# Kernel tuning notes

Hardware: AMD Instinct MI355X
Metric: run time of the kernel (lower is better)

## Reference

```python
import jax, jax.numpy as jnp
import numpy as np
from jax import lax

C = 256        # CONV_DIM / hidden size
VOC = 97       # VOC_SIZE + 1
T_DEC = 25     # NUM_CHARS
N = 512        # number of rois
H_IN, W_IN = 8, 32
GROUPS = 32    # GroupNorm groups (detectron2 'GN' default)


def setup_inputs() -> dict:
    key = jax.random.key(0)
    ks = jax.random.split(key, 16)
    nrm = lambda k, shp, s=0.05: jax.random.normal(k, shp, dtype=jnp.float32) * s
    inp = {}
    inp['rois'] = jax.random.normal(ks[0], (N, C, H_IN, W_IN), dtype=jnp.float32)
    inp['targets'] = jax.random.randint(ks[1], (N, T_DEC), 0, VOC)
    inp['conv1_w'] = nrm(ks[2], (C, C, 3, 3))
    inp['gn1_s'] = jnp.ones((C,), jnp.float32); inp['gn1_b'] = jnp.zeros((C,), jnp.float32)
    inp['conv2_w'] = nrm(ks[3], (C, C, 3, 3))
    inp['gn2_s'] = jnp.ones((C,), jnp.float32); inp['gn2_b'] = jnp.zeros((C,), jnp.float32)
    inp['lstm_wih_f'] = nrm(ks[4], (4 * C, C)); inp['lstm_whh_f'] = nrm(ks[5], (4 * C, C))
    inp['lstm_bih_f'] = jnp.zeros((4 * C,), jnp.float32); inp['lstm_bhh_f'] = jnp.zeros((4 * C,), jnp.float32)
    inp['lstm_wih_b'] = nrm(ks[6], (4 * C, C)); inp['lstm_whh_b'] = nrm(ks[7], (4 * C, C))
    inp['lstm_bih_b'] = jnp.zeros((4 * C,), jnp.float32); inp['lstm_bhh_b'] = jnp.zeros((4 * C,), jnp.float32)
    inp['emb_w'] = nrm(ks[8], (C, 2 * C)); inp['emb_b'] = jnp.zeros((C,), jnp.float32)
    inp['att_emb'] = nrm(ks[9], (VOC, C), 1.0)
    inp['comb_w'] = nrm(ks[10], (C, 2 * C)); inp['comb_b'] = jnp.zeros((C,), jnp.float32)
    inp['gru_wih'] = nrm(ks[11], (3 * C, C)); inp['gru_whh'] = nrm(ks[12], (3 * C, C))
    inp['gru_bih'] = jnp.zeros((3 * C,), jnp.float32); inp['gru_bhh'] = jnp.zeros((3 * C,), jnp.float32)
    inp['out_w'] = nrm(ks[13], (VOC, C)); inp['out_b'] = jnp.zeros((VOC,), jnp.float32)
    inp['vat_w'] = nrm(ks[14], (1, C)); inp['vat_b'] = jnp.zeros((1,), jnp.float32)
    return inp


def group_norm(x, scale, bias, groups=GROUPS, eps=1e-5):
    n, c, h, w = x.shape
    xg = x.reshape(n, groups, c // groups, h, w)
    mu = xg.mean(axis=(2, 3, 4), keepdims=True)
    var = xg.var(axis=(2, 3, 4), keepdims=True)
    xg = (xg - mu) * lax.rsqrt(var + eps)
    return xg.reshape(n, c, h, w) * scale[None, :, None, None] + bias[None, :, None, None]


def lstm_dir(xs, w_ih, w_hh, b_ih, b_hh, reverse):
    # xs: (T, N, C); PyTorch LSTM gate order i, f, g, o
    n = xs.shape[1]; hdim = w_hh.shape[1]
    def step(carry, x):
        h, c = carry
        g = x @ w_ih.T + b_ih + h @ w_hh.T + b_hh
        i, f, gg, o = jnp.split(g, 4, axis=-1)
        c = jax.nn.sigmoid(f) * c + jax.nn.sigmoid(i) * jnp.tanh(gg)
        h = jax.nn.sigmoid(o) * jnp.tanh(c)
        return (h, c), h
    z = jnp.zeros((n, hdim), xs.dtype)
    _, hs = lax.scan(step, (z, z), xs, reverse=reverse)
    return hs


def reference(rois, targets, conv1_w, gn1_s, gn1_b, conv2_w, gn2_s, gn2_b,
              lstm_wih_f, lstm_whh_f, lstm_bih_f, lstm_bhh_f,
              lstm_wih_b, lstm_whh_b, lstm_bih_b, lstm_bhh_b,
              emb_w, emb_b, att_emb, comb_w, comb_b,
              gru_wih, gru_whh, gru_bih, gru_bhh, out_w, out_b, vat_w, vat_b):
    # ---- CRNN encoder ----
    def conv_gn_relu(x, w, s, b):
        y = lax.conv_general_dilated(x, w, window_strides=(2, 1),
                                     padding=((1, 1), (1, 1)),
                                     dimension_numbers=('NCHW', 'OIHW', 'NCHW'))
        return jax.nn.relu(group_norm(y, s, b))
    x = conv_gn_relu(rois, conv1_w, gn1_s, gn1_b)
    x = conv_gn_relu(x, conv2_w, gn2_s, gn2_b)
    x = x.mean(axis=2).transpose(2, 0, 1)            # (T=W, N, C)
    hf = lstm_dir(x, lstm_wih_f, lstm_whh_f, lstm_bih_f, lstm_bhh_f, False)
    hb = lstm_dir(x, lstm_wih_b, lstm_whh_b, lstm_bih_b, lstm_bhh_b, True)
    enc = jnp.concatenate([hf, hb], axis=-1) @ emb_w.T + emb_b   # (T, N, C)

    # ---- attention GRU decoder (training path, deterministic teacher forcing) ----
    n = enc.shape[1]
    dec_in = jnp.concatenate([jnp.zeros((n, 1), targets.dtype), targets[:, :-1]], axis=1).T  # (T_DEC, N)
    dec_tgt = targets.T                                                                        # (T_DEC, N)

    def dec_step(h, inp):
        tok, tgt = inp                       # (N,), (N,)
        emb = att_emb[tok]                   # (N, C); dropout disabled
        alpha = jnp.tanh(h[None] + enc)      # (T, N, C)
        scores = jnp.einsum('tnc,c->tn', alpha, vat_w[0]) + vat_b[0]
        aw = jax.nn.softmax(scores, axis=0)  # softmax over encoder time
        ctx = jnp.einsum('tn,tnc->nc', aw, enc)
        xin = jax.nn.relu(jnp.concatenate([emb, ctx], axis=1) @ comb_w.T + comb_b)
        gi = xin @ gru_wih.T + gru_bih
        gh = h @ gru_whh.T + gru_bhh
        ir, iz, inn = jnp.split(gi, 3, axis=1)
        hr, hz, hn = jnp.split(gh, 3, axis=1)
        r = jax.nn.sigmoid(ir + hr)
        z = jax.nn.sigmoid(iz + hz)
        ng = jnp.tanh(inn + r * hn)
        h_new = (1.0 - z) * ng + z * h
        logp = jax.nn.log_softmax(h_new @ out_w.T + out_b, axis=1)
        step_loss = -jnp.mean(jnp.take_along_axis(logp, tgt[:, None], axis=1))
        return h_new, step_loss

    h0 = jnp.zeros((n, C), enc.dtype)
    _, losses = lax.scan(dec_step, h0, (dec_in, dec_tgt))
    return losses.sum()
```

## Files before the change

kernel.cpp:

```cpp
#include <hip/hip_runtime.h>
#include <math.h>

#define NROI 512
#define CDIM 256
#define TENC 32
#define TDEC 25
#define VOCC 97

typedef unsigned short ushort_t;
typedef unsigned char uchar_t;
typedef __attribute__((ext_vector_type(8))) short short8v;
typedef __attribute__((ext_vector_type(4))) float float4v;

__device__ __forceinline__ float sigmoidf_(float x){
    x = fminf(fmaxf(x, -30.f), 30.f);
    return __builtin_amdgcn_rcpf(1.f + __expf(-x));
}
__device__ __forceinline__ float tanhf_(float x){
    x = fminf(fmaxf(x, -15.f), 15.f);
    float e = __expf(2.f * x);
    return (e - 1.f) * __builtin_amdgcn_rcpf(e + 1.f);
}
__device__ __forceinline__ ushort_t f2b(float f){
    unsigned u = __float_as_uint(f);
    u = u + 0x7fffu + ((u >> 16) & 1u);
    return (ushort_t)(u >> 16);
}
__device__ __forceinline__ float b2f(ushort_t h){
    return __uint_as_float(((unsigned)h) << 16);
}
__device__ __forceinline__ uchar_t f2fp8(float x){
    x = fminf(fmaxf(x, -448.f), 448.f);
    int p = __builtin_amdgcn_cvt_pk_fp8_f32(x, x, 0, false);
    return (uchar_t)(p & 0xff);
}

__global__ void convert_all_k(
    const float* c1s, const float* c2s, const float* wf, const float* wb,
    const float* hf, const float* hb, const float* em, const float* cb,
    const float* gi, const float* gh, const float* ow, const float* ob,
    const float* bif, const float* bhf, const float* bib, const float* bhb,
    ushort_t* d_c1, ushort_t* d_c2, ushort_t* d_wf, ushort_t* d_wb,
    uchar_t* d_hf8, uchar_t* d_hb8, ushort_t* d_em,
    ushort_t* d_cwL, uchar_t* d_cwR8,
    uchar_t* d_gi8, uchar_t* d_gh8, ushort_t* d_ow, float* d_ob,
    float* d_b2f, float* d_b2b)
{
    int i = blockIdx.x * 256 + threadIdx.x;
    if (i < 589824) {
        int co = i / 2304, rem = i % 2304, tap = rem >> 8, ci = rem & 255;
        d_c1[i] = f2b(c1s[co * 2304 + ci * 9 + tap]); return;
    }
    i -= 589824;
    if (i < 589824) {
        int co = i / 2304, rem = i % 2304, tap = rem >> 8, ci = rem & 255;
        d_c2[i] = f2b(c2s[co * 2304 + ci * 9 + tap]); return;
    }
    i -= 589824;
    if (i < 262144) { d_wf[i] = f2b(wf[i]); return; }  i -= 262144;
    if (i < 262144) { d_wb[i] = f2b(wb[i]); return; }  i -= 262144;
    if (i < 262144) { d_hf8[i] = f2fp8(hf[i]); return; }  i -= 262144;
    if (i < 262144) { d_hb8[i] = f2fp8(hb[i]); return; }  i -= 262144;
    if (i < 131072) { d_em[i] = f2b(em[i]); return; }  i -= 131072;
    if (i < 131072) {
        int col = i >> 9, rest = i & 511;
        float v = cb[i];
        if (rest < 256) d_cwL[col * 256 + rest] = f2b(v);
        else            d_cwR8[col * 256 + (rest - 256)] = f2fp8(v);
        return;
    }
    i -= 131072;
    if (i < 196608) { d_gi8[i] = f2fp8(gi[i]); return; }  i -= 196608;
    if (i < 196608) { d_gh8[i] = f2fp8(gh[i]); return; }  i -= 196608;
    if (i < 32768) {
        int r = i >> 8;
        d_ow[i] = (r < VOCC) ? f2b(ow[i - (r << 8) + r * 256]) : 0; return;
    }
    i -= 32768;
    if (i < 128) { d_ob[i] = (i < VOCC) ? ob[i] : 0.f; return; }  i -= 128;
    if (i < 1024) { d_b2f[i] = bif[i] + bhf[i]; return; }  i -= 1024;
    if (i < 1024) { d_b2b[i] = bib[i] + bhb[i]; return; }
}

__global__ void nchw2nhwc_k(const float* __restrict__ in, ushort_t* __restrict__ out)
{
    __shared__ float t[64][33];
    int b = blockIdx.x;
    int cb = b & 3, h = (b >> 2) & 7, n = b >> 5;
    const float* src = in + (((size_t)n * 256 + cb * 64) * 8 + h) * 32;
    int w = threadIdx.x & 31, cr = threadIdx.x >> 5;
    #pragma unroll
    for (int p = 0; p < 8; p++) {
        int c = p * 8 + cr;
        t[c][w] = src[(size_t)c * 256 + w];
    }
    __syncthreads();
    int c2 = threadIdx.x & 63, wr2 = threadIdx.x >> 6;
    ushort_t* dst = out + ((size_t)n * 8 + h) * 32 * 256 + cb * 64;
    #pragma unroll
    for (int q = 0; q < 8; q++) {
        int ww = q * 4 + wr2;
        dst[(size_t)ww * 256 + c2] = f2b(t[c2][ww]);
    }
}

__global__ void emb_gather_k(const int* __restrict__ targets, const float* __restrict__ att_emb,
                             ushort_t* __restrict__ EMB)
{
    int idx = blockIdx.x * 256 + threadIdx.x;
    int c = idx & 255;
    int n = (idx >> 8) & 511;
    int t = idx >> 17;
    int tok = (t == 0) ? 0 : targets[n * TDEC + t - 1];
    EMB[idx] = f2b(att_emb[tok * 256 + c]);
}

template<int OUTBF, int ACT>
__global__ void __launch_bounds__(256, 2)
mgemm_k(const ushort_t* __restrict__ A, const ushort_t* __restrict__ B,
        const float* __restrict__ bias, void* __restrict__ Cout,
        int M, int N, int K)
{
    __shared__ ushort_t As[128 * 40];
    __shared__ ushort_t Bs[128 * 40];
    const int tid = threadIdx.x;
    const int lane = tid & 63, wid = tid >> 6;
    const int wr = wid >> 1, wc = wid & 1;
    const int bm = blockIdx.y * 128, bn = blockIdx.x * 128;

    const int r0 = tid >> 2, c0 = tid & 3;
    const int r1 = r0 + 64;
    const size_t Ar0 = (size_t)(bm + r0) * K, Ar1 = (size_t)(bm + r1) * K;
    const size_t Br0 = (size_t)(bn + r0) * K, Br1 = (size_t)(bn + r1) * K;

    float4v acc[4][4];
    #pragma unroll
    for (int m = 0; m < 4; m++)
        #pragma unroll
        for (int n = 0; n < 4; n++) { float4v z = {0.f,0.f,0.f,0.f}; acc[m][n] = z; }

    short8v ra[2][2], rb[2][2];
    auto LOAD = [&](int b, int k0) {
        ra[b][0] = *(const short8v*)&A[Ar0 + k0 + c0 * 8];
        ra[b][1] = *(const short8v*)&A[Ar1 + k0 + c0 * 8];
        rb[b][0] = *(const short8v*)&B[Br0 + k0 + c0 * 8];
        rb[b][1] = *(const short8v*)&B[Br1 + k0 + c0 * 8];
    };
    auto STORE = [&](int b) {
        *(short8v*)&As[r0 * 40 + c0 * 8] = ra[b][0];
        *(short8v*)&As[r1 * 40 + c0 * 8] = ra[b][1];
        *(short8v*)&Bs[r0 * 40 + c0 * 8] = rb[b][0];
        *(short8v*)&Bs[r1 * 40 + c0 * 8] = rb[b][1];
    };
    const int lr = lane & 15, lk = lane >> 4;
    auto COMPUTE = [&]() {
        short8v af[4], bf[4];
        #pragma unroll
        for (int m = 0; m < 4; m++)
            af[m] = *(const short8v*)&As[(wr * 64 + m * 16 + lr) * 40 + lk * 8];
        #pragma unroll
        for (int n = 0; n < 4; n++)
            bf[n] = *(const short8v*)&Bs[(wc * 64 + n * 16 + lr) * 40 + lk * 8];
        #pragma unroll
        for (int m = 0; m < 4; m++)
            #pragma unroll
            for (int n = 0; n < 4; n++)
                acc[m][n] = __builtin_amdgcn_mfma_f32_16x16x32_bf16(af[m], bf[n], acc[m][n], 0, 0, 0);
    };

    LOAD(0, 0);
    for (int k0 = 0; k0 < K; k0 += 64) {
        __syncthreads();
        STORE(0);
        __syncthreads();
        LOAD(1, k0 + 32);
        COMPUTE();
        __syncthreads();
        STORE(1);
        __syncthreads();
        if (k0 + 64 < K) LOAD(0, k0 + 64);
        COMPUTE();
    }

    #pragma unroll
    for (int m = 0; m < 4; m++)
        #pragma unroll
        for (int n = 0; n < 4; n++)
            #pragma unroll
            for (int r = 0; r < 4; r++) {
                int row = bm + wr * 64 + m * 16 + lk * 4 + r;
                int col = bn + wc * 64 + n * 16 + lr;
                float v = acc[m][n][r];
                if (bias) v += bias[col];
                if (ACT == 1) v = fmaxf(v, 0.f);
                if (OUTBF) ((ushort_t*)Cout)[(size_t)row * N + col] = f2b(v);
                else       ((float*)   Cout)[(size_t)row * N + col] = v;
            }
}

template<int CONV2>
__global__ void __launch_bounds__(256, 2)
convf_k(const ushort_t* __restrict__ in, const ushort_t* __restrict__ wt,
        const float* __restrict__ gns, const float* __restrict__ gnb,
        ushort_t* __restrict__ out, int Hin, int hmask, int nshift)
{
    const int K = 2304;
    __shared__ ushort_t As[128 * 40];
    __shared__ ushort_t Bs[256 * 40];
    const int tid = threadIdx.x;
    const int lane = tid & 63, wv = tid >> 6;
    const int byy = (blockIdx.y & 7) * (gridDim.y >> 3) + (blockIdx.y >> 3);
    const int bm = byy * 128;

    const int r0 = tid >> 2, c0 = tid & 3;
    const int r1 = r0 + 64;
    const int row0 = bm + r0, row1 = bm + r1;
    const int wo0 = row0 & 31, wo1 = row1 & 31;
    const int hh0 = ((row0 >> 5) & hmask) * 2 - 1, hh1 = ((row1 >> 5) & hmask) * 2 - 1;
    const size_t base0 = (size_t)(row0 >> nshift) * Hin * 32 * 256;
    const size_t base1 = (size_t)(row1 >> nshift) * Hin * 32 * 256;
    size_t Br[4];
    #pragma unroll
    for (int j = 0; j < 4; j++) Br[j] = (size_t)(r0 + j * 64) * K;

    float4v acc[8][4];
    #pragma unroll
    for (int m = 0; m < 8; m++)
        #pragma unroll
        for (int n = 0; n < 4; n++) { float4v z = {0.f,0.f,0.f,0.f}; acc[m][n] = z; }

    short8v ra[2][2], rb[2][4];
    const short8v zv = {0,0,0,0,0,0,0,0};
    auto LOAD = [&](int b, int k0) {
        int tap = k0 >> 8;
        int kh = tap / 3, kw = tap - kh * 3;
        int ci = (k0 & 255) + c0 * 8;
        int hi0 = hh0 + kh, wi0 = wo0 - 1 + kw;
        int hi1 = hh1 + kh, wi1 = wo1 - 1 + kw;
        ra[b][0] = ((unsigned)hi0 < (unsigned)Hin && (unsigned)wi0 < 32u)
                 ? *(const short8v*)&in[base0 + ((size_t)hi0 * 32 + wi0) * 256 + ci] : zv;
        ra[b][1] = ((unsigned)hi1 < (unsigned)Hin && (unsigned)wi1 < 32u)
                 ? *(const short8v*)&in[base1 + ((size_t)hi1 * 32 + wi1) * 256 + ci] : zv;
        #pragma unroll
        for (int j = 0; j < 4; j++)
            rb[b][j] = *(const short8v*)&wt[Br[j] + k0 + c0 * 8];
    };
    auto STORE = [&](int b) {
        *(short8v*)&As[r0 * 40 + c0 * 8] = ra[b][0];
        *(short8v*)&As[r1 * 40 + c0 * 8] = ra[b][1];
        #pragma unroll
        for (int j = 0; j < 4; j++)
            *(short8v*)&Bs[(r0 + j * 64) * 40 + c0 * 8] = rb[b][j];
    };
    const int lr = lane & 15, lk = lane >> 4;
    auto COMPUTE = [&]() {
        short8v af[8];
        #pragma unroll
        for (int m = 0; m < 8; m++)
            af[m] = *(const short8v*)&As[(m * 16 + lr) * 40 + lk * 8];
        #pragma unroll
        for (int n = 0; n < 4; n++) {
            short8v bf = *(const short8v*)&Bs[(wv * 64 + n * 16 + lr) * 40 + lk * 8];
            #pragma unroll
            for (int m = 0; m < 8; m++)
                acc[m][n] = __builtin_amdgcn_mfma_f32_16x16x32_bf16(af[m], bf, acc[m][n], 0, 0, 0);
        }
    };

    LOAD(0, 0);
    for (int k0 = 0; k0 < K; k0 += 64) {
        __syncthreads();
        STORE(0);
        __syncthreads();
        LOAD(1, k0 + 32);
        COMPUTE();
        __syncthreads();
        STORE(1);
        __syncthreads();
        if (k0 + 64 < K) LOAD(0, k0 + 64);
        COMPUTE();
    }

    float sc_[4], bb_[4];
    #pragma unroll
    for (int nn = 0; nn < 4; nn++) {
        int col = wv * 64 + nn * 16 + lr;
        sc_[nn] = gns[col];
        bb_[nn] = gnb[col];
    }

    if (CONV2 == 0) {
        float mu_[4], rs_[4];
        #pragma unroll
        for (int nn = 0; nn < 4; nn++) {
            float s = 0.f, q = 0.f;
            #pragma unroll
            for (int m = 0; m < 8; m++)
                #pragma unroll
                for (int r = 0; r < 4; r++) { float v = acc[m][nn][r]; s += v; q += v * v; }
            s += __shfl_xor(s, 16); q += __shfl_xor(q, 16);
            s += __shfl_xor(s, 32); q += __shfl_xor(q, 32);
            s += __shfl_xor(s, 1);  q += __shfl_xor(q, 1);
            s += __shfl_xor(s, 2);  q += __shfl_xor(q, 2);
            s += __shfl_xor(s, 4);  q += __shfl_xor(q, 4);
            float mu = s * (1.f / 1024.f);
            mu_[nn] = mu;
            rs_[nn] = rsqrtf(q * (1.f / 1024.f) - mu * mu + 1e-5f);
        }
        #pragma unroll
        for (int m = 0; m < 8; m++)
            #pragma unroll
            for (int nn = 0; nn < 4; nn++)
                #pragma unroll
                for (int r = 0; r < 4; r++) {
                    int row = bm + m * 16 + lk * 4 + r;
                    int col = wv * 64 + nn * 16 + lr;
                    float v = (acc[m][nn][r] - mu_[nn]) * rs_[nn] * sc_[nn] + bb_[nn];
                    out[(size_t)row * 256 + col] = f2b(fmaxf(v, 0.f));
                }
    } else {
        float mu_[2][4], rs_[2][4];
        #pragma unroll
        for (int img = 0; img < 2; img++)
            #pragma unroll
            for (int nn = 0; nn < 4; nn++) {
                float s = 0.f, q = 0.f;
                #pragma unroll
                for (int m2 = 0; m2 < 4; m2++)
                    #pragma unroll
                    for (int r = 0; r < 4; r++) {
                        float v = acc[img * 4 + m2][nn][r]; s += v; q += v * v;
                    }
                s += __shfl_xor(s, 16); q += __shfl_xor(q, 16);
                s += __shfl_xor(s, 32); q += __shfl_xor(q, 32);
                s += __shfl_xor(s, 1);  q += __shfl_xor(q, 1);
                s += __shfl_xor(s, 2);  q += __shfl_xor(q, 2);
                s += __shfl_xor(s, 4);  q += __shfl_xor(q, 4);
                float mu = s * (1.f / 512.f);
                mu_[img][nn] = mu;
                rs_[img][nn] = rsqrtf(q * (1.f / 512.f) - mu * mu + 1e-5f);
            }
        const int nimg0 = bm >> 6;
        #pragma unroll
        for (int img = 0; img < 2; img++)
            #pragma unroll
            for (int m2 = 0; m2 < 2; m2++)
                #pragma unroll
                for (int nn = 0; nn < 4; nn++)
                    #pragma unroll
                    for (int r = 0; r < 4; r++) {
                        int m = img * 4 + m2;
                        float v0 = (acc[m][nn][r]     - mu_[img][nn]) * rs_[img][nn] * sc_[nn] + bb_[nn];
                        float v1 = (acc[m + 2][nn][r] - mu_[img][nn]) * rs_[img][nn] * sc_[nn] + bb_[nn];
                        float pooled = 0.5f * (fmaxf(v0, 0.f) + fmaxf(v1, 0.f));
                        int wo = m2 * 16 + lk * 4 + r;
                        int nimg = nimg0 + img;
                        int col = wv * 64 + nn * 16 + lr;
                        out[((size_t)wo * 512 + nimg) * 256 + col] = f2b(pooled);
                    }
    }
}

__global__ void __launch_bounds__(512, 1)
lstm_persist_k(const ushort_t* __restrict__ XG,
               const uchar_t* __restrict__ whF8, const uchar_t* __restrict__ whB8,
               ushort_t* __restrict__ hcat)
{
    __shared__ __align__(16) uchar_t hf8[16][264];
    __shared__ float gL[16][1028];
    const int blk = blockIdx.x;
    const int dir = blk >> 5;
    const int r0  = (blk & 31) * 16;
    const uchar_t* W = dir ? whB8 : whF8;
    const int tid = threadIdx.x, lane = tid & 63, wv = tid >> 6;
    const int lr = lane & 15, lk = lane >> 4;
    const float4v z4 = {0.f, 0.f, 0.f, 0.f};

    long pw[8][8];
    #pragma unroll
    for (int j = 0; j < 8; j++) {
        int col0 = (j * 8 + wv) * 16;
        #pragma unroll
        for (int kf = 0; kf < 8; kf++)
            pw[j][kf] = *(const long*)&W[(size_t)(col0 + lr) * 256 + kf * 32 + lk * 8];
    }

    for (int i = tid; i < 16 * 264; i += 512) ((uchar_t*)hf8)[i] = 0;
    float creg[8];
    #pragma unroll
    for (int r = 0; r < 8; r++) creg[r] = 0.f;
    const int ccol = tid & 255;
    const int rbase = (tid >> 8) * 8;
    __syncthreads();

    for (int s = 0; s < TENC; s++) {
        int t = dir ? (31 - s) : s;
        float xga[8][4];
        #pragma unroll
        for (int j = 0; j < 8; j++) {
            int col = (j * 8 + wv) * 16 + lr;
            #pragma unroll
            for (int r = 0; r < 4; r++)
                xga[j][r] = b2f(XG[(size_t)t * 1048576 +
                                   (size_t)(r0 + lk * 4 + r) * 2048 + dir * 1024 + col]);
        }
        long aH[8];
        #pragma unroll
        for (int kf = 0; kf < 8; kf++)
            aH[kf] = *(const long*)&hf8[lr][kf * 32 + lk * 8];
        #pragma unroll
        for (int j = 0; j < 8; j++) {
            int col = (j * 8 + wv) * 16 + lr;
            float4v acc = z4;
            #pragma unroll
            for (int kf = 0; kf < 8; kf++)
                acc = __builtin_amdgcn_mfma_f32_16x16x32_fp8_fp8(aH[kf], pw[j][kf], acc, 0, 0, 0);
            #pragma unroll
            for (int r = 0; r < 4; r++)
                gL[lk * 4 + r][col] = acc[r] + xga[j][r];
        }
        __syncthreads();
        #pragma unroll
        for (int rr = 0; rr < 8; rr++) {
            int row = rbase + rr;
            float i_ = sigmoidf_(gL[row][ccol]);
            float f_ = sigmoidf_(gL[row][256 + ccol]);
            float g_ = tanhf_(gL[row][512 + ccol]);
            float o_ = sigmoidf_(gL[row][768 + ccol]);
            float cn = f_ * creg[rr] + i_ * g_;
            creg[rr] = cn;
            float hn = o_ * tanhf_(cn);
            hf8[row][ccol] = f2fp8(hn);
            hcat[((size_t)t * 512 + (r0 + row)) * 512 + dir * 256 + ccol] = f2b(hn);
        }
        __syncthreads();
    }
}

__global__ void __launch_bounds__(512, 1)
dec_local_k(const ushort_t* __restrict__ enc, const ushort_t* __restrict__ xinpre,
            const uchar_t* __restrict__ cwR8, const uchar_t* __restrict__ gwih8,
            const uchar_t* __restrict__ gwhh8, const float* __restrict__ gbih,
            const float* __restrict__ gbhh, const float* __restrict__ vw,
            const float* __restrict__ vb, ushort_t* __restrict__ hist)
{
    __shared__ ushort_t encL[2][32][264];
    __shared__ __align__(16) uchar_t cwL8[16 * 8 * 64 * 8];
    __shared__ float    hL[2][256];
    __shared__ __align__(16) uchar_t hf8[2][264];
    __shared__ __align__(16) uchar_t xf8[2][264];
    __shared__ __align__(16) uchar_t ctx8[2][264];
    __shared__ float    giL[2][776];
    __shared__ float    ghL[2][776];
    __shared__ float    scl[2][32];

    const int tid = threadIdx.x, lane = tid & 63, wv = tid >> 6;
    const int nbase = blockIdx.x * 2;
    const int lr = lane & 15, lk = lane >> 4;
    const float4v z4 = {0.f,0.f,0.f,0.f};

    for (int i = tid; i < 2 * 256; i += 512) hL[i >> 8][i & 255] = 0.f;
    for (int i = tid; i < 2 * 264; i += 512) hf8[i / 264][i % 264] = 0;
    for (int v = tid; v < 2048; v += 512) {
        int r = v >> 10;
        int rem = v & 1023;
        int t2 = rem >> 5;
        int c8 = (rem & 31) * 8;
        *(short8v*)&encL[r][t2][c8] =
            *(const short8v*)&enc[((size_t)t2 * 512 + nbase + r) * 256 + c8];
    }
    #pragma unroll
    for (int q = 0; q < 2; q++) {
        int tile = wv * 2 + q;
        int col0 = tile * 16;
        #pragma unroll
        for (int kf = 0; kf < 8; kf++) {
            long v = *(const long*)&cwR8[(size_t)(col0 + lr) * 256 + kf * 32 + lk * 8];
            *(long*)&cwL8[((tile * 8 + kf) * 64 + lane) * 8] = v;
        }
    }
    long pgh[6][8], pgi[6][8];
    #pragma unroll
    for (int j = 0; j < 6; j++) {
        int col0 = (j * 8 + wv) * 16;
        #pragma unroll
        for (int kf = 0; kf < 8; kf++) {
            pgh[j][kf] = *(const long*)&gwhh8[(size_t)(col0 + lr) * 256 + kf * 32 + lk * 8];
            pgi[j][kf] = *(const long*)&gwih8[(size_t)(col0 + lr) * 256 + kf * 32 + lk * 8];
        }
    }
    __syncthreads();

    float vwreg[4];
    #pragma unroll
    for (int j = 0; j < 4; j++) vwreg[j] = vw[lane + 64 * j];
    const float vbias = vb[0];
    float gbh_r[6], gbi_r[6];
    #pragma unroll
    for (int j = 0; j < 6; j++) {
        int col0 = (j * 8 + wv) * 16;
        gbh_r[j] = gbhh[col0 + lr];
        gbi_r[j] = gbih[col0 + lr];
    }

    for (int t = 0; t < TDEC; t++) {
        float xp[2][2];
        #pragma unroll
        for (int q = 0; q < 2; q++) {
            int col0 = (wv * 2 + q) * 16;
            xp[q][0] = b2f(xinpre[(size_t)t * 131072 + (size_t)(nbase + 0) * 256 + col0 + lr]);
            xp[q][1] = b2f(xinpre[(size_t)t * 131072 + (size_t)(nbase + 1) * 256 + col0 + lr]);
        }
        float4v ghacc[6];
        {
            long aH[8];
            #pragma unroll
            for (int kf = 0; kf < 8; kf++)
                aH[kf] = (lr < 2) ? *(const long*)&hf8[lr][kf * 32 + lk * 8] : 0L;
            #pragma unroll
            for (int j = 0; j < 6; j++) {
                float4v acc = z4;
                #pragma unroll
                for (int kf = 0; kf < 8; kf++)
                    acc = __builtin_amdgcn_mfma_f32_16x16x32_fp8_fp8(aH[kf], pgh[j][kf], acc, 0, 0, 0);
                ghacc[j] = acc;
            }
        }
        {
            int r = wv >> 2;
            int t2b = (wv & 3) * 8;
            float hreg[4];
            #pragma unroll
            for (int j = 0; j < 4; j++) hreg[j] = hL[r][lane + 64 * j];
            #pragma unroll
            for (int q = 0; q < 8; q++) {
                int t2 = t2b + q;
                float s = 0.f;
                #pragma unroll
                for (int j = 0; j < 4; j++)
                    s += tanhf_(hreg[j] + b2f(encL[r][t2][lane + 64 * j])) * vwreg[j];
                for (int o = 32; o > 0; o >>= 1) s += __shfl_down(s, o);
                if (lane == 0) scl[r][t2] = s + vbias;
            }
        }
        if (lk == 0) {
            #pragma unroll
            for (int j = 0; j < 6; j++) {
                int col0 = (j * 8 + wv) * 16;
                ghL[0][col0 + lr] = ghacc[j][0] + gbh_r[j];
                ghL[1][col0 + lr] = ghacc[j][1] + gbh_r[j];
            }
        }
        __syncthreads();
        {
            int r = tid >> 8, c = tid & 255;
            float m = -1e30f;
            #pragma unroll
            for (int t2 = 0; t2 < 32; t2++) m = fmaxf(m, scl[r][t2]);
            float ssum = 0.f, acc = 0.f;
            #pragma unroll 8
            for (int t2 = 0; t2 < 32; t2++) {
                float e = __expf(scl[r][t2] - m);
                ssum += e;
                acc += e * b2f(encL[r][t2][c]);
            }
            ctx8[r][c] = f2fp8(acc * __builtin_amdgcn_rcpf(ssum));
        }
        __syncthreads();
        {
            long aC[8];
            #pragma unroll
            for (int kf = 0; kf < 8; kf++)
                aC[kf] = (lr < 2) ? *(const long*)&ctx8[lr][kf * 32 + lk * 8] : 0L;
            #pragma unroll
            for (int q = 0; q < 2; q++) {
                int tile = wv * 2 + q;
                int col0 = tile * 16;
                float4v acc = z4;
                #pragma unroll
                for (int kf = 0; kf < 8; kf++) {
                    long b = *(const long*)&cwL8[((tile * 8 + kf) * 64 + lane) * 8];
                    acc = __builtin_amdgcn_mfma_f32_16x16x32_fp8_fp8(aC[kf], b, acc, 0, 0, 0);
                }
                if (lk == 0) {
                    xf8[0][col0 + lr] = f2fp8(fmaxf(acc[0] + xp[q][0], 0.f));
                    xf8[1][col0 + lr] = f2fp8(fmaxf(acc[1] + xp[q][1], 0.f));
                }
            }
        }
        __syncthreads();
        {
            long aX[8];
            #pragma unroll
            for (int kf = 0; kf < 8; kf++)
                aX[kf] = (lr < 2) ? *(const long*)&xf8[lr][kf * 32 + lk * 8] : 0L;
            #pragma unroll
            for (int j = 0; j < 6; j++) {
                int col0 = (j * 8 + wv) * 16;
                float4v acc = z4;
                #pragma unroll
                for (int kf = 0; kf < 8; kf++)
                    acc = __builtin_amdgcn_mfma_f32_16x16x32_fp8_fp8(aX[kf], pgi[j][kf], acc, 0, 0, 0);
                if (lk == 0) {
                    giL[0][col0 + lr] = acc[0] + gbi_r[j];
                    giL[1][col0 + lr] = acc[1] + gbi_r[j];
                }
            }
        }
        __syncthreads();
        {
            int r = tid >> 8, c = tid & 255;
            float rg = sigmoidf_(giL[r][c] + ghL[r][c]);
            float zg = sigmoidf_(giL[r][256 + c] + ghL[r][256 + c]);
            float ng = tanhf_(giL[r][512 + c] + rg * ghL[r][512 + c]);
            float hv = (1.f - zg) * ng + zg * hL[r][c];
            hL[r][c] = hv;
            hf8[r][c] = f2fp8(hv);
            __builtin_nontemporal_store(f2b(hv), &hist[((size_t)t * 512 + nbase + r) * 256 + c]);
        }
        __syncthreads();
    }
}

__global__ void loss_batch_k(const float* __restrict__ logits, const int* __restrict__ targets,
                             float* __restrict__ part)
{
    __shared__ float red[256];
    int t = blockIdx.x;
    float acc = 0.f;
    for (int rr = threadIdx.x; rr < 512; rr += 256) {
        const float* row = logits + ((size_t)t * 512 + rr) * 128;
        float m = -1e30f;
        for (int j = 0; j < VOCC; j++) m = fmaxf(m, row[j]);
        float s2 = 0.f;
        for (int j = 0; j < VOCC; j++) s2 += __expf(row[j] - m);
        int tg = targets[rr * TDEC + t];
        acc += m + __logf(s2) - row[tg];
    }
    red[threadIdx.x] = acc;
    __syncthreads();
    for (int o = 128; o > 0; o >>= 1) {
        if (threadIdx.x < o) red[threadIdx.x] += red[threadIdx.x + o];
        __syncthreads();
    }
    if (threadIdx.x == 0) part[t] = red[0] / 512.f;
}

__global__ void loss_final_k(const float* __restrict__ part, float* __restrict__ out)
{
    if (threadIdx.x == 0) {
        float s = 0.f;
        for (int t = 0; t < TDEC; t++) s += part[t];
        out[0] = s;
    }
}

extern "C" void kernel_launch(void* const* d_in, const int* in_sizes, int n_in,
                              void* d_out, int out_size, void* d_ws, size_t ws_size,
                              hipStream_t stream)
{
    const float* rois     = (const float*)d_in[0];
    const int*   targets  = (const int*)  d_in[1];
    const float* conv1_w  = (const float*)d_in[2];
    const float* gn1_s    = (const float*)d_in[3];
    const float* gn1_b    = (const float*)d_in[4];
    const float* conv2_w  = (const float*)d_in[5];
    const float* gn2_s    = (const float*)d_in[6];
    const float* gn2_b    = (const float*)d_in[7];
    const float* wih_f    = (const float*)d_in[8];
    const float* whh_f    = (const float*)d_in[9];
    const float* bih_f    = (const float*)d_in[10];
    const float* bhh_f    = (const float*)d_in[11];
    const float* wih_b    = (const float*)d_in[12];
    const float* whh_b    = (const float*)d_in[13];
    const float* bih_b    = (const float*)d_in[14];
    const float* bhh_b    = (const float*)d_in[15];
    const float* emb_w    = (const float*)d_in[16];
    const float* emb_b    = (const float*)d_in[17];
    const float* att_emb  = (const float*)d_in[18];
    const float* comb_w   = (const float*)d_in[19];
    const float* comb_b   = (const float*)d_in[20];
    const float* gru_wih  = (const float*)d_in[21];
    const float* gru_whh  = (const float*)d_in[22];
    const float* gru_bih  = (const float*)d_in[23];
    const float* gru_bhh  = (const float*)d_in[24];
    const float* out_w    = (const float*)d_in[25];
    const float* out_b    = (const float*)d_in[26];
    const float* vat_w    = (const float*)d_in[27];
    const float* vat_b    = (const float*)d_in[28];

    float* ws = (float*)d_ws;
    const size_t REG1 = 0;
    const size_t REG2 = 16777216;
    const size_t REG3 = 25165824;
    const size_t WREG = 33554432;

    ushort_t* R      = (ushort_t*)(ws + REG1);
    ushort_t* xg     = (ushort_t*)(ws + REG1);
    ushort_t* EMB    = (ushort_t*)(ws + REG1);
    ushort_t* xinpre = (ushort_t*)(ws + REG1 + 1638400);

    ushort_t* xT     = (ushort_t*)(ws + REG2 + 4194304);
    ushort_t* hcat   = (ushort_t*)(ws + REG2);
    ushort_t* X1b    = (ushort_t*)(ws + REG3);
    ushort_t* enc    = (ushort_t*)(ws + REG3);
    ushort_t* hist   = (ushort_t*)(ws + REG3 + 2097152);
    float*    logitsA= ws + REG3 + 3735552;
    float*    lpart  = ws + REG3 + 5373952;

    ushort_t* c1w    = (ushort_t*)(ws + WREG);
    ushort_t* c2w    = (ushort_t*)(ws + WREG + 294912);
    ushort_t* wihf   = (ushort_t*)(ws + WREG + 589824);
    uchar_t*  whhf8  = (uchar_t*) (ws + WREG + 851968);
    uchar_t*  whhb8  = (uchar_t*) (ws + WREG + 917504);
    ushort_t* embw   = (ushort_t*)(ws + WREG + 1114112);
    ushort_t* cwL    = (ushort_t*)(ws + WREG + 1179648);
    uchar_t*  cwR8   = (uchar_t*) (ws + WREG + 1212416);
    uchar_t*  gwih8  = (uchar_t*) (ws + WREG + 1245184);
    uchar_t*  gwhh8  = (uchar_t*) (ws + WREG + 1294336);
    ushort_t* outw   = (ushort_t*)(ws + WREG + 1343488);
    float*    outb   = ws + WREG + 1359872;
    float*    bias2f = ws + WREG + 1360000;
    float*    bias2b = ws + WREG + 1361024;

    dim3 blk(256);

    convert_all_k<<<11402, blk, 0, stream>>>(
        conv1_w, conv2_w, wih_f, wih_b, whh_f, whh_b, emb_w, comb_w,
        gru_wih, gru_whh, out_w, out_b, bih_f, bhh_f, bih_b, bhh_b,
        c1w, c2w, wihf, (ushort_t*)(ws + WREG + 720896), whhf8, whhb8, embw,
        cwL, cwR8, gwih8, gwhh8, outw, outb, bias2f, bias2b);

    nchw2nhwc_k<<<16384, blk, 0, stream>>>(rois, R);
    convf_k<0><<<dim3(1, 512), blk, 0, stream>>>(R, c1w, gn1_s, gn1_b, X1b, 8, 3, 7);
    convf_k<1><<<dim3(1, 256), blk, 0, stream>>>(X1b, c2w, gn2_s, gn2_b, xT, 4, 1, 6);

    mgemm_k<1,0><<<dim3(16, 128), blk, 0, stream>>>(xT, wihf, bias2f, xg, 16384, 2048, 256);

    lstm_persist_k<<<64, dim3(512), 0, stream>>>(xg, whhf8, whhb8, hcat);

    mgemm_k<1,0><<<dim3(2, 128), blk, 0, stream>>>(hcat, embw, emb_b, enc, 16384, 256, 512);

    emb_gather_k<<<12800, blk, 0, stream>>>(targets, att_emb, EMB);
    mgemm_k<1,0><<<dim3(2, 100), blk, 0, stream>>>(EMB, cwL, comb_b, xinpre, 12800, 256, 256);

    dec_local_k<<<256, dim3(512), 0, stream>>>(enc, xinpre, cwR8, gwih8, gwhh8,
        gru_bih, gru_bhh, vat_w, vat_b, hist);

    mgemm_k<0,0><<<dim3(1, 100), blk, 0, stream>>>(hist, outw, outb, logitsA, 12800, 128, 256);
    loss_batch_k<<<TDEC, blk, 0, stream>>>(logitsA, targets, lpart);
    loss_final_k<<<1, dim3(64), 0, stream>>>(lpart, (float*)d_out);
}
```

Measured before the change: 719.3 us.

## Spread LSTM and GRU decoder recurrences over more blocks with fewer rows each

The persistent LSTM kernel now handles 4 ROI rows per block across 256 blocks instead of 16 rows across 64 blocks. The GRU attention decoder now handles one ROI per block across 512 blocks instead of two per block across 256. The goal is to cut the length of each block's serial recurrence and spread the work over more compute units of the MI355X. In exchange, each MFMA tile carries more zero padding, half the threads sit idle in the elementwise phases, and every block reloads the recurrent weights into registers, which adds more weight traffic overall. The decoder's launch bound changes from (512,1) to (512,4), which could force register spilling given the large per-thread weight arrays.

Measured after the change: 775.7 us. +7.8%, slower.

```diff
diff --git a/kernel.cpp b/kernel.cpp
--- a/kernel.cpp
+++ b/kernel.cpp
@@ -366,11 +366,11 @@
                const uchar_t* __restrict__ whF8, const uchar_t* __restrict__ whB8,
                ushort_t* __restrict__ hcat)
 {
-    __shared__ __align__(16) uchar_t hf8[16][264];
-    __shared__ float gL[16][1028];
+    __shared__ __align__(16) uchar_t hf8[4][264];
+    __shared__ float gL[4][1028];
     const int blk = blockIdx.x;
-    const int dir = blk >> 5;
-    const int r0  = (blk & 31) * 16;
+    const int dir = blk >> 7;
+    const int r0  = (blk & 127) * 4;
     const uchar_t* W = dir ? whB8 : whF8;
     const int tid = threadIdx.x, lane = tid & 63, wv = tid >> 6;
     const int lr = lane & 15, lk = lane >> 4;
@@ -385,29 +385,30 @@
             pw[j][kf] = *(const long*)&W[(size_t)(col0 + lr) * 256 + kf * 32 + lk * 8];
     }
 
-    for (int i = tid; i < 16 * 264; i += 512) ((uchar_t*)hf8)[i] = 0;
-    float creg[8];
-    #pragma unroll
-    for (int r = 0; r < 8; r++) creg[r] = 0.f;
+    for (int i = tid; i < 4 * 264; i += 512) ((uchar_t*)hf8)[i] = 0;
+    float creg[2];
+    creg[0] = 0.f; creg[1] = 0.f;
     const int ccol = tid & 255;
-    const int rbase = (tid >> 8) * 8;
+    const int rbase = (tid >> 8) * 2;
     __syncthreads();
 
     for (int s = 0; s < TENC; s++) {
         int t = dir ? (31 - s) : s;
         float xga[8][4];
-        #pragma unroll
-        for (int j = 0; j < 8; j++) {
-            int col = (j * 8 + wv) * 16 + lr;
-            #pragma unroll
-            for (int r = 0; r < 4; r++)
-                xga[j][r] = b2f(XG[(size_t)t * 1048576 +
-                                   (size_t)(r0 + lk * 4 + r) * 2048 + dir * 1024 + col]);
+        if (lk == 0) {
+            #pragma unroll
+            for (int j = 0; j < 8; j++) {
+                int col = (j * 8 + wv) * 16 + lr;
+                #pragma unroll
+                for (int r = 0; r < 4; r++)
+                    xga[j][r] = b2f(XG[(size_t)t * 1048576 +
+                                       (size_t)(r0 + r) * 2048 + dir * 1024 + col]);
+            }
         }
         long aH[8];
         #pragma unroll
         for (int kf = 0; kf < 8; kf++)
-            aH[kf] = *(const long*)&hf8[lr][kf * 32 + lk * 8];
+            aH[kf] = (lr < 4) ? *(const long*)&hf8[lr][kf * 32 + lk * 8] : 0L;
         #pragma unroll
         for (int j = 0; j < 8; j++) {
             int col = (j * 8 + wv) * 16 + lr;
@@ -415,13 +416,15 @@
             #pragma unroll
             for (int kf = 0; kf < 8; kf++)
                 acc = __builtin_amdgcn_mfma_f32_16x16x32_fp8_fp8(aH[kf], pw[j][kf], acc, 0, 0, 0);
-            #pragma unroll
-            for (int r = 0; r < 4; r++)
-                gL[lk * 4 + r][col] = acc[r] + xga[j][r];
-        }
-        __syncthreads();
-        #pragma unroll
-        for (int rr = 0; rr < 8; rr++) {
+            if (lk == 0) {
+                #pragma unroll
+                for (int r = 0; r < 4; r++)
+                    gL[r][col] = acc[r] + xga[j][r];
+            }
+        }
+        __syncthreads();
+        #pragma unroll
+        for (int rr = 0; rr < 2; rr++) {
             int row = rbase + rr;
             float i_ = sigmoidf_(gL[row][ccol]);
             float f_ = sigmoidf_(gL[row][256 + ccol]);
@@ -437,37 +440,35 @@
     }
 }
 
-__global__ void __launch_bounds__(512, 1)
+__global__ void __launch_bounds__(512, 4)
 dec_local_k(const ushort_t* __restrict__ enc, const ushort_t* __restrict__ xinpre,
             const uchar_t* __restrict__ cwR8, const uchar_t* __restrict__ gwih8,
             const uchar_t* __restrict__ gwhh8, const float* __restrict__ gbih,
             const float* __restrict__ gbhh, const float* __restrict__ vw,
             const float* __restrict__ vb, ushort_t* __restrict__ hist)
 {
-    __shared__ ushort_t encL[2][32][264];
+    __shared__ ushort_t encL[32][264];
     __shared__ __align__(16) uchar_t cwL8[16 * 8 * 64 * 8];
-    __shared__ float    hL[2][256];
-    __shared__ __align__(16) uchar_t hf8[2][264];
-    __shared__ __align__(16) uchar_t xf8[2][264];
-    __shared__ __align__(16) uchar_t ctx8[2][264];
-    __shared__ float    giL[2][776];
-    __shared__ float    ghL[2][776];
-    __shared__ float    scl[2][32];
+    __shared__ float    hL[256];
+    __shared__ __align__(16) uchar_t hf8[264];
+    __shared__ __align__(16) uchar_t xf8[264];
+    __shared__ __align__(16) uchar_t ctx8[264];
+    __shared__ float    giL[776];
+    __shared__ float    ghL[776];
+    __shared__ float    scl[32];
 
     const int tid = threadIdx.x, lane = tid & 63, wv = tid >> 6;
-    const int nbase = blockIdx.x * 2;
+    const int n = blockIdx.x;
     const int lr = lane & 15, lk = lane >> 4;
     const float4v z4 = {0.f,0.f,0.f,0.f};
 
-    for (int i = tid; i < 2 * 256; i += 512) hL[i >> 8][i & 255] = 0.f;
-    for (int i = tid; i < 2 * 264; i += 512) hf8[i / 264][i % 264] = 0;
-    for (int v = tid; v < 2048; v += 512) {
-        int r = v >> 10;
-        int rem = v & 1023;
-        int t2 = rem >> 5;
-        int c8 = (rem & 31) * 8;
-        *(short8v*)&encL[r][t2][c8] =
-            *(const short8v*)&enc[((size_t)t2 * 512 + nbase + r) * 256 + c8];
+    for (int i = tid; i < 256; i += 512) hL[i] = 0.f;
+    for (int i = tid; i < 264; i += 512) hf8[i] = 0;
+    for (int v = tid; v < 1024; v += 512) {
+        int t2 = v >> 5;
+        int c8 = (v & 31) * 8;
+        *(short8v*)&encL[t2][c8] =
+            *(const short8v*)&enc[((size_t)t2 * 512 + n) * 256 + c8];
     }
     #pragma unroll
     for (int q = 0; q < 2; q++) {
@@ -504,19 +505,18 @@
     }
 
     for (int t = 0; t < TDEC; t++) {
-        float xp[2][2];
+        float xp[2];
         #pragma unroll
         for (int q = 0; q < 2; q++) {
             int col0 = (wv * 2 + q) * 16;
-            xp[q][0] = b2f(xinpre[(size_t)t * 131072 + (size_t)(nbase + 0) * 256 + col0 + lr]);
-            xp[q][1] = b2f(xinpre[(size_t)t * 131072 + (size_t)(nbase + 1) * 256 + col0 + lr]);
+            xp[q] = b2f(xinpre[(size_t)t * 131072 + (size_t)n * 256 + col0 + lr]);
         }
         float4v ghacc[6];
         {
             long aH[8];
             #pragma unroll
             for (int kf = 0; kf < 8; kf++)
-                aH[kf] = (lr < 2) ? *(const long*)&hf8[lr][kf * 32 + lk * 8] : 0L;
+                aH[kf] = (lr == 0) ? *(const long*)&hf8[kf * 32 + lk * 8] : 0L;
             #pragma unroll
             for (int j = 0; j < 6; j++) {
                 float4v acc = z4;
@@ -527,51 +527,49 @@
             }
         }
         {
-            int r = wv >> 2;
-            int t2b = (wv & 3) * 8;
+            int t2b = wv * 4;
             float hreg[4];
             #pragma unroll
-            for (int j = 0; j < 4; j++) hreg[j] = hL[r][lane + 64 * j];
-            #pragma unroll
-            for (int q = 0; q < 8; q++) {
+            for (int j = 0; j < 4; j++) hreg[j] = hL[lane + 64 * j];
+            #pragma unroll
+            for (int q = 0; q < 4; q++) {
                 int t2 = t2b + q;
                 float s = 0.f;
                 #pragma unroll
                 for (int j = 0; j < 4; j++)
-                    s += tanhf_(hreg[j] + b2f(encL[r][t2][lane + 64 * j])) * vwreg[j];
+                    s += tanhf_(hreg[j] + b2f(encL[t2][lane + 64 * j])) * vwreg[j];
                 for (int o = 32; o > 0; o >>= 1) s += __shfl_down(s, o);
-                if (lane == 0) scl[r][t2] = s + vbias;
+                if (lane == 0) scl[t2] = s + vbias;
             }
         }
         if (lk == 0) {
             #pragma unroll
             for (int j = 0; j < 6; j++) {
                 int col0 = (j * 8 + wv) * 16;
-                ghL[0][col0 + lr] = ghacc[j][0] + gbh_r[j];
-                ghL[1][col0 + lr] = ghacc[j][1] + gbh_r[j];
-            }
-        }
-        __syncthreads();
-        {
-            int r = tid >> 8, c = tid & 255;
+                ghL[col0 + lr] = ghacc[j][0] + gbh_r[j];
+            }
+        }
+        __syncthreads();
+        if (tid < 256) {
+            int c = tid;
             float m = -1e30f;
             #pragma unroll
-            for (int t2 = 0; t2 < 32; t2++) m = fmaxf(m, scl[r][t2]);
+            for (int t2 = 0; t2 < 32; t2++) m = fmaxf(m, scl[t2]);
             float ssum = 0.f, acc = 0.f;
             #pragma unroll 8
             for (int t2 = 0; t2 < 32; t2++) {
-                float e = __expf(scl[r][t2] - m);
+                float e = __expf(scl[t2] - m);
                 ssum += e;
-                acc += e * b2f(encL[r][t2][c]);
-            }
-            ctx8[r][c] = f2fp8(acc * __builtin_amdgcn_rcpf(ssum));
+                acc += e * b2f(encL[t2][c]);
+            }
+            ctx8[c] = f2fp8(acc * __builtin_amdgcn_rcpf(ssum));
         }
         __syncthreads();
         {
             long aC[8];
             #pragma unroll
             for (int kf = 0; kf < 8; kf++)
-                aC[kf] = (lr < 2) ? *(const long*)&ctx8[lr][kf * 32 + lk * 8] : 0L;
+                aC[kf] = (lr == 0) ? *(const long*)&ctx8[kf * 32 + lk * 8] : 0L;
             #pragma unroll
             for (int q = 0; q < 2; q++) {
                 int tile = wv * 2 + q;
@@ -582,10 +580,8 @@
                     long b = *(const long*)&cwL8[((tile * 8 + kf) * 64 + lane) * 8];
                     acc = __builtin_amdgcn_mfma_f32_16x16x32_fp8_fp8(aC[kf], b, acc, 0, 0, 0);
                 }
-                if (lk == 0) {
-                    xf8[0][col0 + lr] = f2fp8(fmaxf(acc[0] + xp[q][0], 0.f));
-                    xf8[1][col0 + lr] = f2fp8(fmaxf(acc[1] + xp[q][1], 0.f));
-                }
+                if (lk == 0)
+                    xf8[col0 + lr] = f2fp8(fmaxf(acc[0] + xp[q], 0.f));
             }
         }
         __syncthreads();
@@ -593,7 +589,7 @@
             long aX[8];
             #pragma unroll
             for (int kf = 0; kf < 8; kf++)
-                aX[kf] = (lr < 2) ? *(const long*)&xf8[lr][kf * 32 + lk * 8] : 0L;
+                aX[kf] = (lr == 0) ? *(const long*)&xf8[kf * 32 + lk * 8] : 0L;
             #pragma unroll
             for (int j = 0; j < 6; j++) {
                 int col0 = (j * 8 + wv) * 16;
@@ -601,22 +597,20 @@
                 #pragma unroll
                 for (int kf = 0; kf < 8; kf++)
                     acc = __builtin_amdgcn_mfma_f32_16x16x32_fp8_fp8(aX[kf], pgi[j][kf], acc, 0, 0, 0);
-                if (lk == 0) {
-                    giL[0][col0 + lr] = acc[0] + gbi_r[j];
-                    giL[1][col0 + lr] = acc[1] + gbi_r[j];
-                }
-            }
-        }
-        __syncthreads();
-        {
-            int r = tid >> 8, c = tid & 255;
-            float rg = sigmoidf_(giL[r][c] + ghL[r][c]);
-            float zg = sigmoidf_(giL[r][256 + c] + ghL[r][256 + c]);
-            float ng = tanhf_(giL[r][512 + c] + rg * ghL[r][512 + c]);
-            float hv = (1.f - zg) * ng + zg * hL[r][c];
-            hL[r][c] = hv;
-            hf8[r][c] = f2fp8(hv);
-            __builtin_nontemporal_store(f2b(hv), &hist[((size_t)t * 512 + nbase + r) * 256 + c]);
+                if (lk == 0)
+                    giL[col0 + lr] = acc[0] + gbi_r[j];
+            }
+        }
+        __syncthreads();
+        if (tid < 256) {
+            int c = tid;
+            float rg = sigmoidf_(giL[c] + ghL[c]);
+            float zg = sigmoidf_(giL[256 + c] + ghL[256 + c]);
+            float ng = tanhf_(giL[512 + c] + rg * ghL[512 + c]);
+            float hv = (1.f - zg) * ng + zg * hL[c];
+            hL[c] = hv;
+            hf8[c] = f2fp8(hv);
+            __builtin_nontemporal_store(f2b(hv), &hist[((size_t)t * 512 + n) * 256 + c]);
         }
         __syncthreads();
     }
@@ -737,14 +731,14 @@
 
     mgemm_k<1,0><<<dim3(16, 128), blk, 0, stream>>>(xT, wihf, bias2f, xg, 16384, 2048, 256);
 
-    lstm_persist_k<<<64, dim3(512), 0, stream>>>(xg, whhf8, whhb8, hcat);
+    lstm_persist_k<<<256, dim3(512), 0, stream>>>(xg, whhf8, whhb8, hcat);
 
     mgemm_k<1,0><<<dim3(2, 128), blk, 0, stream>>>(hcat, embw, emb_b, enc, 16384, 256, 512);
 
     emb_gather_k<<<12800, blk, 0, stream>>>(targets, att_emb, EMB);
     mgemm_k<1,0><<<dim3(2, 100), blk, 0, stream>>>(EMB, cwL, comb_b, xinpre, 12800, 256, 256);
 
-    dec_local_k<<<256, dim3(512), 0, stream>>>(enc, xinpre, cwR8, gwih8, gwhh8,
+    dec_local_k<<<512, dim3(512), 0, stream>>>(enc, xinpre, cwR8, gwih8, gwhh8,
         gru_bih, gru_bhh, vat_w, vat_b, hist);
 
     mgemm_k<0,0><<<dim3(1, 100), blk, 0, stream>>>(hist, outw, outb, logitsA, 12800, 128, 256);
```
